# Kernel optimization log

Hardware: AMD Instinct MI355X
Metric: run time of the kernel (lower is better)

Reference implementation:

```python
import jax, jax.numpy as jnp
import numpy as np

B, S, M = 8, 2048, 256
D = 512          # input/memory feature dim
P = 512          # proj_dim
H = 8            # num_heads


def setup_inputs() -> dict:
    key = jax.random.key(0)
    ks = jax.random.split(key, 10)
    sc = 0.02
    return {
        "input_seq": jax.random.normal(ks[0], (B, S, D), jnp.float32),
        "memory_cells": jax.random.normal(ks[1], (B, M, D), jnp.float32),
        "Wk": jax.random.normal(ks[2], (D, P), jnp.float32) * sc,
        "bk": jnp.zeros((P,), jnp.float32),
        "Wv": jax.random.normal(ks[3], (D, P), jnp.float32) * sc,
        "bv": jnp.zeros((P,), jnp.float32),
        "Wq": jax.random.normal(ks[4], (H, D, P), jnp.float32) * sc,  # stacked per-head query Dense
        "bq": jnp.zeros((H, P), jnp.float32),
        "Wo": jax.random.normal(ks[5], (H * P, P), jnp.float32) * sc,
        "bo": jnp.zeros((P,), jnp.float32),
    }


def reference(input_seq, memory_cells, Wk, bk, Wv, bv, Wq, bq, Wo, bo):
    # shared key/value projections (multi-query: one K/V for all heads)
    ik = input_seq @ Wk + bk          # [B,S,P]
    mk = memory_cells @ Wk + bk       # [B,M,P]
    iv = input_seq @ Wv + bv          # [B,S,P]
    mv = memory_cells @ Wv + bv       # [B,M,P]

    # per-head queries from memory cells, all heads at once
    q = jnp.einsum('bmd,hdp->bhmp', memory_cells, Wq) + bq[None, :, None, :]  # [B,H,M,P]

    input_score = jnp.einsum('bhmp,bsp->bhms', q, ik)          # [B,H,M,S]
    self_score = jnp.sum(q * mk[:, None], axis=-1, keepdims=True)  # [B,H,M,1]
    score = jnp.concatenate([self_score, input_score], axis=-1)    # [B,H,M,S+1]
    score = score / jnp.sqrt(jnp.float32(P))
    attn = jax.nn.softmax(score, axis=-1)

    self_attn = attn[..., 0:1]                                  # [B,H,M,1]
    input_attn = attn[..., 1:]                                  # [B,H,M,S]
    val = jnp.einsum('bhms,bsp->bhmp', input_attn, iv) + self_attn * mv[:, None]

    # concat heads: [B,M,H*P]
    concat = jnp.transpose(val, (0, 2, 1, 3)).reshape(B, M, H * P)
    return concat @ Wo + bo           # [B,M,P]
```

## Files before the change

### kernel.cpp

```cpp
#include <hip/hip_runtime.h>

#define B_ 8
#define S_ 2048
#define M_ 256
#define D_ 512
#define P_ 512
#define H_ 8

#define SCALE 0.044194173824159216f

typedef __attribute__((ext_vector_type(8))) short bf16x8;
typedef __attribute__((ext_vector_type(4))) float f32x4;

static __device__ __forceinline__ float bf2f(short u) {
  union { float f; unsigned int i; } x;
  x.i = ((unsigned int)(unsigned short)u) << 16;
  return x.f;
}
static __device__ __forceinline__ short f2bf(float f) {
  union { float f; unsigned int i; } x;
  x.f = f;
  unsigned int r = (x.i + 0x7FFFu + ((x.i >> 16) & 1u)) >> 16;
  return (short)r;
}

static __device__ __forceinline__ void gll16(const short* g, short* l) {
  __builtin_amdgcn_global_load_lds(
      (const __attribute__((address_space(1))) void*)g,
      (__attribute__((address_space(3))) void*)l, 16, 0, 0);
}

#define LGKM_WAIT() asm volatile("s_waitcnt lgkmcnt(0)" ::: "memory")

__global__ __launch_bounds__(256) void cast_both(
    const float* __restrict__ inA, short* __restrict__ outA, int n4A,
    const float* __restrict__ inM, short* __restrict__ outM)
{
  int idx = blockIdx.x * 256 + threadIdx.x;
  const float* in = inA;
  short* out = outA;
  if (idx >= n4A) { idx -= n4A; in = inM; out = outM; }
  float4 v = ((const float4*)in)[idx];
  short o0 = f2bf(v.x), o1 = f2bf(v.y), o2 = f2bf(v.z), o3 = f2bf(v.w);
  uint2 pk;
  pk.x = (unsigned int)(unsigned short)o0 | ((unsigned int)(unsigned short)o1 << 16);
  pk.y = (unsigned int)(unsigned short)o2 | ((unsigned int)(unsigned short)o3 << 16);
  ((uint2*)out)[idx] = pk;
}

__global__ __launch_bounds__(256) void wtrans_all(
    const float* __restrict__ Wk, const float* __restrict__ Wv,
    const float* __restrict__ Wq,
    short* __restrict__ WkT, short* __restrict__ WvT, short* __restrict__ WqT)
{
  __shared__ float tile[32][33];
  const int t = threadIdx.x, tx = t & 31, ty = t >> 5;
  const int z = blockIdx.z;
  const float* inp;
  short* outp;
  if (z == 0)      { inp = Wk; outp = WkT; }
  else if (z == 1) { inp = Wv; outp = WvT; }
  else             { inp = Wq + (size_t)(z - 2) * 512 * 512;
                     outp = WqT + (size_t)(z - 2) * 512 * 512; }
  const int n0 = blockIdx.x * 32, k0 = blockIdx.y * 32;
#pragma unroll
  for (int i = 0; i < 4; ++i)
    tile[ty + 8 * i][tx] = inp[(size_t)(k0 + ty + 8 * i) * 512 + n0 + tx];
  __syncthreads();
#pragma unroll
  for (int i = 0; i < 4; ++i)
    outp[(size_t)(n0 + ty + 8 * i) * 512 + k0 + tx] = f2bf(tile[tx][ty + 8 * i]);
}

__global__ __launch_bounds__(256) void wtrans_wo(
    const float* __restrict__ in, short* __restrict__ out)
{
  __shared__ float tile[32][33];
  const int t = threadIdx.x, tx = t & 31, ty = t >> 5;
  const int n0 = blockIdx.x * 32, k0 = blockIdx.y * 32;
#pragma unroll
  for (int i = 0; i < 4; ++i)
    tile[ty + 8 * i][tx] = in[(size_t)(k0 + ty + 8 * i) * 512 + n0 + tx];
  __syncthreads();
#pragma unroll
  for (int i = 0; i < 4; ++i)
    out[(size_t)(n0 + ty + 8 * i) * 4096 + k0 + tx] = f2bf(tile[tx][ty + 8 * i]);
}

template<int MODE, int K, int N, int LDA, int LDB>
__global__ __launch_bounds__(256, 3) void gemm128(
    const short* __restrict__ Abase, const short* __restrict__ Bbase,
    const float* __restrict__ bias, void* __restrict__ Cv,
    const size_t aZ, const size_t bZ, const size_t cZ,
    float* __restrict__ Ls,
    const float* __restrict__ eselfp, const short* __restrict__ mvbp)
{
  __shared__ short As[4096];
  __shared__ short Bs[4096];
  const int t = threadIdx.x;
  const int w = t >> 6, lane = t & 63, qd = lane >> 4, ln = lane & 15;
  const int wm = (w & 1) * 64, wn = (w >> 1) * 64;

  int z, m0, n0, bsel;
  if constexpr (MODE == 2 || MODE == 3) {
    const int b = blockIdx.x;
    n0 = blockIdx.y * 128;
    const int h = blockIdx.z & 7, mb = blockIdx.z >> 3;
    z = b * 8 + h;
    m0 = mb * 128;
    bsel = b;
  } else {
    n0 = blockIdx.x * 128;
    m0 = blockIdx.y * 128;
    z = blockIdx.z;
    bsel = z;
  }

  const short* A  = Abase + (size_t)z * aZ;
  const short* Bp = Bbase + (size_t)bsel * bZ;

  const int rr = t >> 2, g0 = t & 3;
  const int gs0 = g0 ^ ((rr >> 1) & 3);
  const int gs1 = g0 ^ (((rr + 64) >> 1) & 3);
  const short* ga0 = A + (size_t)(m0 + rr) * LDA + gs0 * 8;
  const short* ga1 = A + (size_t)(m0 + rr + 64) * LDA + gs1 * 8;
  const short* gb0 = Bp + (size_t)(n0 + rr) * LDB + gs0 * 8;
  const short* gb1 = Bp + (size_t)(n0 + rr + 64) * LDB + gs1 * 8;

  int aoff[4], boff[4];
#pragma unroll
  for (int mt = 0; mt < 4; ++mt) {
    int r = wm + mt * 16 + ln;
    aoff[mt] = r * 32 + (qd ^ ((r >> 1) & 3)) * 8;
  }
#pragma unroll
  for (int nt = 0; nt < 4; ++nt) {
    int r = wn + nt * 16 + ln;
    boff[nt] = r * 32 + (qd ^ ((r >> 1) & 3)) * 8;
  }

  f32x4 acc[4][4];
#pragma unroll
  for (int mt = 0; mt < 4; ++mt)
#pragma unroll
    for (int nt = 0; nt < 4; ++nt) acc[mt][nt] = (f32x4){0.f, 0.f, 0.f, 0.f};

  for (int kc = 0; kc < K; kc += 32) {
    __syncthreads();
    gll16(ga0 + kc, &As[w * 512]);
    gll16(ga1 + kc, &As[2048 + w * 512]);
    gll16(gb0 + kc, &Bs[w * 512]);
    gll16(gb1 + kc, &Bs[2048 + w * 512]);
    __syncthreads();

    bf16x8 af[4], bfr[4];
#pragma unroll
    for (int mt = 0; mt < 4; ++mt) af[mt] = *(const bf16x8*)&As[aoff[mt]];
#pragma unroll
    for (int nt = 0; nt < 4; ++nt) bfr[nt] = *(const bf16x8*)&Bs[boff[nt]];
#pragma unroll
    for (int mt = 0; mt < 4; ++mt)
#pragma unroll
      for (int nt = 0; nt < 4; ++nt)
        acc[mt][nt] = __builtin_amdgcn_mfma_f32_16x16x32_bf16(af[mt], bfr[nt], acc[mt][nt], 0, 0, 0);
  }

  if constexpr (MODE == 5) {
#pragma unroll
    for (int nt = 0; nt < 4; ++nt) {
      const int col = n0 + wn + nt * 16 + ln;
#pragma unroll
      for (int mt = 0; mt < 4; ++mt)
#pragma unroll
        for (int r = 0; r < 4; ++r) {
          const int row = m0 + wm + mt * 16 + qd * 4 + r;
          ((float*)Cv)[(size_t)z * cZ + (size_t)row * N + col] = acc[mt][nt][r];
        }
    }
  } else if constexpr (MODE == 2) {
#pragma unroll
    for (int mt = 0; mt < 4; ++mt)
#pragma unroll
      for (int nt = 0; nt < 4; ++nt)
#pragma unroll
        for (int r = 0; r < 4; ++r)
          acc[mt][nt][r] = __expf(acc[mt][nt][r] * SCALE);
#pragma unroll
    for (int mt = 0; mt < 4; ++mt)
#pragma unroll
      for (int r = 0; r < 4; ++r) {
        float rsum = acc[mt][0][r] + acc[mt][1][r] + acc[mt][2][r] + acc[mt][3][r];
        rsum += __shfl_xor(rsum, 1);
        rsum += __shfl_xor(rsum, 2);
        rsum += __shfl_xor(rsum, 4);
        rsum += __shfl_xor(rsum, 8);
        if (ln == 0) {
          const int row = m0 + wm + mt * 16 + qd * 4 + r;
          atomicAdd(&Ls[(size_t)z * M_ + row], rsum);
        }
      }
#pragma unroll
    for (int nt = 0; nt < 4; ++nt) {
      const int col = n0 + wn + nt * 16 + ln;
#pragma unroll
      for (int mt = 0; mt < 4; ++mt)
#pragma unroll
        for (int r = 0; r < 4; ++r) {
          const int row = m0 + wm + mt * 16 + qd * 4 + r;
          ((short*)Cv)[(size_t)z * cZ + (size_t)row * N + col] = f2bf(acc[mt][nt][r]);
        }
    }
  } else if constexpr (MODE == 3) {
    const int zb = z >> 3, hh = z & 7;
#pragma unroll
    for (int mt = 0; mt < 4; ++mt)
#pragma unroll
      for (int r = 0; r < 4; ++r) {
        const int row = m0 + wm + mt * 16 + qd * 4 + r;
        const float es = eselfp[(size_t)z * M_ + row];
        const float inv = 1.f / (es + Ls[(size_t)z * M_ + row]);
        const short* mvr = mvbp + ((size_t)(zb * M_ + row)) * P_;
        short* outr = (short*)Cv + ((size_t)(zb * M_ + row)) * (H_ * P_) + (size_t)hh * P_;
#pragma unroll
        for (int nt = 0; nt < 4; ++nt) {
          const int col = n0 + wn + nt * 16 + ln;
          outr[col] = f2bf((acc[mt][nt][r] + es * bf2f(mvr[col])) * inv);
        }
      }
  } else {
#pragma unroll
    for (int nt = 0; nt < 4; ++nt) {
      const int col = n0 + wn + nt * 16 + ln;
      const float bc = bias[512 * z + col];
#pragma unroll
      for (int mt = 0; mt < 4; ++mt)
#pragma unroll
        for (int r = 0; r < 4; ++r) {
          const int row = m0 + wm + mt * 16 + qd * 4 + r;
          const int bidx = row >> 8, ml = row & 255;
          ((short*)Cv)[((size_t)(bidx * H_ + z) * M_ + ml) * N + col] = f2bf(acc[mt][nt][r] + bc);
        }
    }
  }
}

template<bool TRANSV>
__global__ __launch_bounds__(256, 3) void proj_kv(
    const short* __restrict__ A,
    const short* __restrict__ WkT, const short* __restrict__ WvT,
    const float* __restrict__ bk, const float* __restrict__ bv,
    short* __restrict__ Ck, short* __restrict__ Cvv)
{
  __shared__ short Sh[8192];
  short* As  = Sh;
  short* Bks = Sh + 4096;
  short* Bvs = Sh + 6144;
  const int t = threadIdx.x;
  const int w = t >> 6, lane = t & 63, qd = lane >> 4, ln = lane & 15;
  const int n0 = blockIdx.x * 64, m0 = blockIdx.y * 128;
  const int wm = (w & 1) * 64, wn2 = (w >> 1) * 32;

  const int rr = t >> 2, g0 = t & 3;
  const int gs0 = g0 ^ ((rr >> 1) & 3);
  const int gs1 = g0 ^ (((rr + 64) >> 1) & 3);
  const short* ga0 = A + (size_t)(m0 + rr) * 512 + gs0 * 8;
  const short* ga1 = A + (size_t)(m0 + rr + 64) * 512 + gs1 * 8;
  const short* gbk = WkT + (size_t)(n0 + rr) * 512 + gs0 * 8;
  const short* gbv = WvT + (size_t)(n0 + rr) * 512 + gs0 * 8;

  int aoff[4], boff[2];
#pragma unroll
  for (int mt = 0; mt < 4; ++mt) {
    int r = wm + mt * 16 + ln;
    aoff[mt] = r * 32 + (qd ^ ((r >> 1) & 3)) * 8;
  }
#pragma unroll
  for (int nt = 0; nt < 2; ++nt) {
    int r = wn2 + nt * 16 + ln;
    boff[nt] = r * 32 + (qd ^ ((r >> 1) & 3)) * 8;
  }

  f32x4 accK[4][2], accV[4][2];
#pragma unroll
  for (int mt = 0; mt < 4; ++mt)
#pragma unroll
    for (int nt = 0; nt < 2; ++nt) {
      accK[mt][nt] = (f32x4){0.f, 0.f, 0.f, 0.f};
      accV[mt][nt] = (f32x4){0.f, 0.f, 0.f, 0.f};
    }

  for (int kc = 0; kc < 512; kc += 32) {
    __syncthreads();
    gll16(ga0 + kc, &As[w * 512]);
    gll16(ga1 + kc, &As[2048 + w * 512]);
    gll16(gbk + kc, &Bks[w * 512]);
    gll16(gbv + kc, &Bvs[w * 512]);
    __syncthreads();

    bf16x8 af[4], bkf[2], bvf[2];
#pragma unroll
    for (int mt = 0; mt < 4; ++mt) af[mt] = *(const bf16x8*)&As[aoff[mt]];
#pragma unroll
    for (int nt = 0; nt < 2; ++nt) {
      bkf[nt] = *(const bf16x8*)&Bks[boff[nt]];
      bvf[nt] = *(const bf16x8*)&Bvs[boff[nt]];
    }
#pragma unroll
    for (int mt = 0; mt < 4; ++mt)
#pragma unroll
      for (int nt = 0; nt < 2; ++nt) {
        accK[mt][nt] = __builtin_amdgcn_mfma_f32_16x16x32_bf16(af[mt], bkf[nt], accK[mt][nt], 0, 0, 0);
        accV[mt][nt] = __builtin_amdgcn_mfma_f32_16x16x32_bf16(af[mt], bvf[nt], accV[mt][nt], 0, 0, 0);
      }
  }

#pragma unroll
  for (int nt = 0; nt < 2; ++nt) {
    const int col = n0 + wn2 + nt * 16 + ln;
    const float bc = bk[col];
#pragma unroll
    for (int mt = 0; mt < 4; ++mt)
#pragma unroll
      for (int r = 0; r < 4; ++r) {
        const int row = m0 + wm + mt * 16 + qd * 4 + r;
        Ck[(size_t)row * 512 + col] = f2bf(accK[mt][nt][r] + bc);
      }
  }

  if constexpr (!TRANSV) {
#pragma unroll
    for (int nt = 0; nt < 2; ++nt) {
      const int col = n0 + wn2 + nt * 16 + ln;
      const float bc = bv[col];
#pragma unroll
      for (int mt = 0; mt < 4; ++mt)
#pragma unroll
        for (int r = 0; r < 4; ++r) {
          const int row = m0 + wm + mt * 16 + qd * 4 + r;
          Cvv[(size_t)row * 512 + col] = f2bf(accV[mt][nt][r] + bc);
        }
    }
  } else {
    __syncthreads();
    short* ep = &Sh[w * 1280];
    const int lr = lane >> 1, lc16 = (lane & 1) * 16;
#pragma unroll
    for (int pass = 0; pass < 2; ++pass) {
#pragma unroll
      for (int mh = 0; mh < 2; ++mh) {
        const int mt = pass * 2 + mh;
#pragma unroll
        for (int nt = 0; nt < 2; ++nt) {
          const float bc = bv[n0 + wn2 + nt * 16 + ln];
#pragma unroll
          for (int r = 0; r < 4; ++r)
            ep[(nt * 16 + ln) * 40 + mh * 16 + qd * 4 + r] = f2bf(accV[mt][nt][r] + bc);
        }
      }
      LGKM_WAIT();
      const int srow0 = m0 + wm + pass * 32;
      const int bidx = srow0 >> 11;
      const int sloc = (srow0 & 2047) + lc16;
      const int pcol = n0 + wn2 + lr;
      short* outp = Cvv + (size_t)bidx * P_ * S_ + (size_t)pcol * S_ + sloc;
      *(bf16x8*)outp = *(const bf16x8*)&ep[lr * 40 + lc16];
      *(bf16x8*)(outp + 8) = *(const bf16x8*)&ep[lr * 40 + lc16 + 8];
      LGKM_WAIT();
    }
  }
}

__global__ __launch_bounds__(256) void reduce_wo(
    const float* __restrict__ partial, const float* __restrict__ bo,
    float* __restrict__ out)
{
  const int idx4 = blockIdx.x * 256 + threadIdx.x;
  float4 s = ((const float4*)bo)[idx4 & 127];
#pragma unroll
  for (int zz = 0; zz < 4; ++zz) {
    float4 p = ((const float4*)partial)[(size_t)zz * 262144 + idx4];
    s.x += p.x; s.y += p.y; s.z += p.z; s.w += p.w;
  }
  ((float4*)out)[idx4] = s;
}

__global__ __launch_bounds__(256) void selfscore(
    const short* __restrict__ qb, const short* __restrict__ mkb,
    float* __restrict__ eself, float* __restrict__ Ls)
{
  const int z = blockIdx.x, t = threadIdx.x;
  const short* qr = qb + ((size_t)z * M_ + t) * P_;
  const short* mr = mkb + ((size_t)(z >> 3) * M_ + t) * P_;
  float s = 0.f;
#pragma unroll 8
  for (int c = 0; c < P_; c += 8) {
    bf16x8 qv = *(const bf16x8*)(qr + c);
    bf16x8 mv = *(const bf16x8*)(mr + c);
#pragma unroll
    for (int j = 0; j < 8; ++j) s += bf2f(qv[j]) * bf2f(mv[j]);
  }
  eself[(size_t)z * M_ + t] = __expf(s * SCALE);
  Ls[(size_t)z * M_ + t] = 0.f;
}

extern "C" void kernel_launch(void* const* d_in, const int* in_sizes, int n_in,
                              void* d_out, int out_size, void* d_ws, size_t ws_size,
                              hipStream_t stream) {
  const float* input_seq = (const float*)d_in[0];
  const float* memcells  = (const float*)d_in[1];
  const float* Wk = (const float*)d_in[2];
  const float* bk = (const float*)d_in[3];
  const float* Wv = (const float*)d_in[4];
  const float* bv = (const float*)d_in[5];
  const float* Wq = (const float*)d_in[6];
  const float* bq = (const float*)d_in[7];
  const float* Wo = (const float*)d_in[8];
  const float* bo = (const float*)d_in[9];
  float* out = (float*)d_out;

  short* ws = (short*)d_ws;
  size_t o = 0;
  short* valb = ws + o; o += (size_t)B_ * M_ * H_ * P_;
  short* WoT  = ws + o; o += (size_t)(H_ * P_) * P_;
  short* mvb  = ws + o; o += (size_t)B_ * M_ * P_;
  short* mkb  = ws + o; o += (size_t)B_ * M_ * P_;
  short* qb   = ws + o; o += (size_t)B_ * H_ * M_ * P_;
  short* ivT  = ws + o; o += (size_t)B_ * P_ * S_;
  short* ikb  = ws + o; o += (size_t)B_ * S_ * P_;
  float* partial = (float*)(ws + o); o += (size_t)B_ * H_ * M_ * P_;
  float* eself = (float*)(ws + o); o += 2 * (size_t)B_ * H_ * M_;
  float* Ls    = (float*)(ws + o); o += 2 * (size_t)B_ * H_ * M_;
  short* region2 = ws + o;
  short* Ab  = region2;
  short* Mb  = Ab + (size_t)B_ * S_ * D_;
  short* WkT = Mb + (size_t)B_ * M_ * D_;
  short* WvT = WkT + (size_t)D_ * P_;
  short* WqT = WvT + (size_t)D_ * P_;
  short* Eb  = region2;

  dim3 blk(256);

  const int n4A = B_ * S_ * D_ / 4;
  const int n4M = B_ * M_ * D_ / 4;
  cast_both<<<dim3((n4A + n4M) / 256), blk, 0, stream>>>(input_seq, Ab, n4A, memcells, Mb);
  wtrans_all<<<dim3(16, 16, 10), blk, 0, stream>>>(Wk, Wv, Wq, WkT, WvT, WqT);
  wtrans_wo<<<dim3(16, 128), blk, 0, stream>>>(Wo, WoT);

  proj_kv<true><<<dim3(8, 128), blk, 0, stream>>>(Ab, WkT, WvT, bk, bv, ikb, ivT);
  proj_kv<false><<<dim3(8, 16), blk, 0, stream>>>(Mb, WkT, WvT, bk, bv, mkb, mvb);

  gemm128<1, 512, 512, 512, 512><<<dim3(4, 16, 8), blk, 0, stream>>>(
      Mb, WqT, bq, qb, 0, (size_t)D_ * P_, 0, nullptr, nullptr, nullptr);

  selfscore<<<dim3(64), blk, 0, stream>>>(qb, mkb, eself, Ls);

  gemm128<2, 512, 2048, 512, 512><<<dim3(8, 16, 16), blk, 0, stream>>>(
      qb, ikb, nullptr, Eb, (size_t)M_ * P_, (size_t)S_ * P_,
      (size_t)M_ * S_, Ls, nullptr, nullptr);

  gemm128<3, 2048, 512, 2048, 2048><<<dim3(8, 4, 16), blk, 0, stream>>>(
      Eb, ivT, nullptr, valb, (size_t)M_ * S_, (size_t)P_ * S_,
      0, Ls, eself, mvb);

  gemm128<5, 1024, 512, 4096, 4096><<<dim3(4, 16, 4), blk, 0, stream>>>(
      valb, WoT, nullptr, partial, 1024, 1024,
      (size_t)2048 * 512, nullptr, nullptr, nullptr);
  reduce_wo<<<dim3(1024), blk, 0, stream>>>(partial, bo, out);
}
```

Before: 323.4 us.

## Use 256x256 tiled 8-wave GEMM with quadrant ping-pong for score and value stages

Adds a new gemm256 kernel (512 threads, 256x256 output tiles, K-tile 64, double-buffered LDS staged through global_load_lds) and uses it for the two attention GEMMs in place of gemm128. Each K-step is split into four MFMA quadrants interleaved with LDS fragment reads, staged global prefetches and raw barriers, with setprio raised around the MFMA bursts. The larger tiles raise operand reuse and cut global traffic. In exchange they use 128KB of LDS and more registers, which lowers occupancy, and the MODE 3 grid shrinks to 128 blocks, which may underfill the GPU.

Result: no change. 325.3 us (+0.6%).

```diff
diff --git a/kernel.cpp b/kernel.cpp
--- a/kernel.cpp
+++ b/kernel.cpp
@@ -31,6 +31,7 @@
 }
 
 #define LGKM_WAIT() asm volatile("s_waitcnt lgkmcnt(0)" ::: "memory")
+#define RAW_BAR() do { asm volatile("" ::: "memory"); __builtin_amdgcn_s_barrier(); asm volatile("" ::: "memory"); } while (0)
 
 __global__ __launch_bounds__(256) void cast_both(
     const float* __restrict__ inA, short* __restrict__ outA, int n4A,
@@ -241,6 +242,181 @@
           ((short*)Cv)[((size_t)(bidx * H_ + z) * M_ + ml) * N + col] = f2bf(acc[mt][nt][r] + bc);
         }
     }
+  }
+}
+
+template<int MH, int NH>
+static __device__ __forceinline__ void mfma_quad(
+    f32x4 (&acc)[8][4], const bf16x8 (&a)[4][2], const bf16x8 (&bfr)[2][2])
+{
+  __builtin_amdgcn_s_setprio(1);
+#pragma unroll
+  for (int kk = 0; kk < 2; ++kk)
+#pragma unroll
+    for (int mt = 0; mt < 4; ++mt)
+#pragma unroll
+      for (int nt = 0; nt < 2; ++nt)
+        acc[MH * 4 + mt][NH * 2 + nt] = __builtin_amdgcn_mfma_f32_16x16x32_bf16(
+            a[mt][kk], bfr[nt][kk], acc[MH * 4 + mt][NH * 2 + nt], 0, 0, 0);
+  __builtin_amdgcn_s_setprio(0);
+}
+
+template<int MODE, int K, int LDA, int LDB>
+__global__ __launch_bounds__(512, 2) void gemm256(
+    const short* __restrict__ Abase, const short* __restrict__ Bbase,
+    void* __restrict__ Cv, float* __restrict__ Ls,
+    const float* __restrict__ eselfp, const short* __restrict__ mvbp,
+    const size_t aZ, const size_t bZ)
+{
+  __shared__ short lds[65536];
+  constexpr int NKT = K / 64;
+  static_assert(NKT >= 2, "need at least 2 K-tiles");
+  const int t = threadIdx.x;
+  const int w = t >> 6, lane = t & 63, qd = lane >> 4, ln = lane & 15;
+  const int wr = w >> 2, wc = w & 3;
+  const int b = blockIdx.x;
+  const int n0 = blockIdx.y * 256, m0 = blockIdx.z * 256;
+
+  const short* A  = Abase + (size_t)b * aZ;
+  const short* Bp = Bbase + (size_t)b * bZ;
+
+  const int s0 = w * 64 + lane, s1 = s0 + 512;
+  const int sr0 = s0 >> 3, sc0 = ((s0 & 7) ^ (sr0 & 7)) * 8;
+  const int sr1 = s1 >> 3, sc1 = ((s1 & 7) ^ (sr1 & 7)) * 8;
+
+  auto stage = [&](const short* gorigin, int ldg, short* lbase) {
+    gll16(gorigin + (size_t)sr0 * ldg + sc0, lbase + w * 512);
+    gll16(gorigin + (size_t)sr1 * ldg + sc1, lbase + 4096 + w * 512);
+  };
+
+  const int cq0 = ((qd    ) ^ (ln & 7)) * 8;
+  const int cq1 = ((4 + qd) ^ (ln & 7)) * 8;
+  const int brow = (wc & 1) * 64;
+
+  f32x4 acc[8][4];
+#pragma unroll
+  for (int i = 0; i < 8; ++i)
+#pragma unroll
+    for (int j = 0; j < 4; ++j) acc[i][j] = (f32x4){0.f, 0.f, 0.f, 0.f};
+
+  stage(A  + (size_t)m0 * LDA,          LDA, &lds[0]);
+  stage(A  + (size_t)(m0 + 128) * LDA,  LDA, &lds[8192]);
+  stage(Bp + (size_t)n0 * LDB,          LDB, &lds[32768]);
+  stage(Bp + (size_t)(n0 + 128) * LDB,  LDB, &lds[32768 + 8192]);
+  stage(Bp + (size_t)n0 * LDB + 64,     LDB, &lds[32768 + 16384]);
+  asm volatile("s_waitcnt vmcnt(2)" ::: "memory");
+  __builtin_amdgcn_s_barrier();
+
+#pragma unroll 1
+  for (int kt = 0; kt < NKT; ++kt) {
+    const int p = kt & 1;
+    short* Ah = &lds[p * 16384 + wr * 8192];
+    short* Bh = &lds[32768 + p * 16384 + (wc >> 1) * 8192];
+    bf16x8 a[4][2], bfr[2][2];
+
+#pragma unroll
+    for (int mt = 0; mt < 4; ++mt) {
+      a[mt][0] = *(const bf16x8*)&Ah[(mt * 16 + ln) * 64 + cq0];
+      a[mt][1] = *(const bf16x8*)&Ah[(mt * 16 + ln) * 64 + cq1];
+    }
+#pragma unroll
+    for (int nt = 0; nt < 2; ++nt) {
+      bfr[nt][0] = *(const bf16x8*)&Bh[(brow + nt * 16 + ln) * 64 + cq0];
+      bfr[nt][1] = *(const bf16x8*)&Bh[(brow + nt * 16 + ln) * 64 + cq1];
+    }
+    if (kt + 1 < NKT) {
+      stage(A  + (size_t)m0 * LDA + (kt + 1) * 64,          LDA, &lds[(p ^ 1) * 16384]);
+      stage(Bp + (size_t)(n0 + 128) * LDB + (kt + 1) * 64,  LDB, &lds[32768 + (p ^ 1) * 16384 + 8192]);
+    }
+    RAW_BAR(); LGKM_WAIT();
+    mfma_quad<0, 0>(acc, a, bfr);
+    RAW_BAR();
+
+#pragma unroll
+    for (int mt = 0; mt < 4; ++mt) {
+      a[mt][0] = *(const bf16x8*)&Ah[4096 + (mt * 16 + ln) * 64 + cq0];
+      a[mt][1] = *(const bf16x8*)&Ah[4096 + (mt * 16 + ln) * 64 + cq1];
+    }
+    if (kt + 1 < NKT)
+      stage(A + (size_t)(m0 + 128) * LDA + (kt + 1) * 64, LDA, &lds[(p ^ 1) * 16384 + 8192]);
+    RAW_BAR(); LGKM_WAIT();
+    mfma_quad<1, 0>(acc, a, bfr);
+    RAW_BAR();
+
+#pragma unroll
+    for (int nt = 0; nt < 2; ++nt) {
+      bfr[nt][0] = *(const bf16x8*)&Bh[(brow + 32 + nt * 16 + ln) * 64 + cq0];
+      bfr[nt][1] = *(const bf16x8*)&Bh[(brow + 32 + nt * 16 + ln) * 64 + cq1];
+    }
+    RAW_BAR(); LGKM_WAIT();
+    mfma_quad<1, 1>(acc, a, bfr);
+    RAW_BAR();
+
+#pragma unroll
+    for (int mt = 0; mt < 4; ++mt) {
+      a[mt][0] = *(const bf16x8*)&Ah[(mt * 16 + ln) * 64 + cq0];
+      a[mt][1] = *(const bf16x8*)&Ah[(mt * 16 + ln) * 64 + cq1];
+    }
+    if (kt + 2 < NKT)
+      stage(Bp + (size_t)n0 * LDB + (kt + 2) * 64, LDB, &lds[32768 + p * 16384]);
+    RAW_BAR(); LGKM_WAIT();
+    mfma_quad<0, 1>(acc, a, bfr);
+    if (kt + 2 < NKT) { asm volatile("s_waitcnt vmcnt(2)" ::: "memory"); }
+    else              { asm volatile("s_waitcnt vmcnt(0)" ::: "memory"); }
+    RAW_BAR();
+  }
+
+  if constexpr (MODE == 2) {
+#pragma unroll
+    for (int i = 0; i < 8; ++i)
+#pragma unroll
+      for (int j = 0; j < 4; ++j)
+#pragma unroll
+        for (int r = 0; r < 4; ++r)
+          acc[i][j][r] = __expf(acc[i][j][r] * SCALE);
+#pragma unroll
+    for (int i = 0; i < 8; ++i)
+#pragma unroll
+      for (int r = 0; r < 4; ++r) {
+        float rs = acc[i][0][r] + acc[i][1][r] + acc[i][2][r] + acc[i][3][r];
+        rs += __shfl_xor(rs, 1);
+        rs += __shfl_xor(rs, 2);
+        rs += __shfl_xor(rs, 4);
+        rs += __shfl_xor(rs, 8);
+        if (ln == 0) {
+          const int row = m0 + wr * 128 + i * 16 + qd * 4 + r;
+          atomicAdd(&Ls[(size_t)b * 2048 + row], rs);
+        }
+      }
+    short* Cb = (short*)Cv + (size_t)b * 2048 * 2048;
+#pragma unroll
+    for (int j = 0; j < 4; ++j) {
+      const int col = n0 + wc * 64 + j * 16 + ln;
+#pragma unroll
+      for (int i = 0; i < 8; ++i)
+#pragma unroll
+        for (int r = 0; r < 4; ++r) {
+          const int row = m0 + wr * 128 + i * 16 + qd * 4 + r;
+          Cb[(size_t)row * 2048 + col] = f2bf(acc[i][j][r]);
+        }
+    }
+  } else {
+#pragma unroll
+    for (int i = 0; i < 8; ++i)
+#pragma unroll
+      for (int r = 0; r < 4; ++r) {
+        const int R = m0 + wr * 128 + i * 16 + qd * 4 + r;
+        const float es  = eselfp[(size_t)b * 2048 + R];
+        const float inv = 1.f / (es + Ls[(size_t)b * 2048 + R]);
+        const int h = R >> 8, m = R & 255;
+        const short* mvr = mvbp + ((size_t)(b * 256 + m)) * 512;
+        short* outr = (short*)Cv + ((size_t)(b * 256 + m)) * 4096 + (size_t)h * 512;
+#pragma unroll
+        for (int j = 0; j < 4; ++j) {
+          const int col = n0 + wc * 64 + j * 16 + ln;
+          outr[col] = f2bf((acc[i][j][r] + es * bf2f(mvr[col])) * inv);
+        }
+      }
   }
 }
 
@@ -454,13 +630,13 @@
 
   selfscore<<<dim3(64), blk, 0, stream>>>(qb, mkb, eself, Ls);
 
-  gemm128<2, 512, 2048, 512, 512><<<dim3(8, 16, 16), blk, 0, stream>>>(
-      qb, ikb, nullptr, Eb, (size_t)M_ * P_, (size_t)S_ * P_,
-      (size_t)M_ * S_, Ls, nullptr, nullptr);
-
-  gemm128<3, 2048, 512, 2048, 2048><<<dim3(8, 4, 16), blk, 0, stream>>>(
-      Eb, ivT, nullptr, valb, (size_t)M_ * S_, (size_t)P_ * S_,
-      0, Ls, eself, mvb);
+  gemm256<2, 512, 512, 512><<<dim3(8, 8, 8), dim3(512), 0, stream>>>(
+      qb, ikb, Eb, Ls, nullptr, nullptr,
+      (size_t)2048 * 512, (size_t)2048 * 512);
+
+  gemm256<3, 2048, 2048, 2048><<<dim3(8, 2, 8), dim3(512), 0, stream>>>(
+      Eb, ivT, valb, Ls, eself, mvb,
+      (size_t)2048 * 2048, (size_t)512 * 2048);
 
   gemm128<5, 1024, 512, 4096, 4096><<<dim3(4, 16, 4), blk, 0, stream>>>(
       valb, WoT, nullptr, partial, 1024, 1024,
```
